# Optimization experiments

Measured on AMD Instinct MI355X. Metric: run time of the kernel, lower is better.

Reference implementation:

```python
import jax, jax.numpy as jnp
import numpy as np

C0 = 32          # cs[0] == cs[1] with planes=[32,32,...], cr=1.0
CIN = 4
EPS = 1e-5

# ---------- host-side coordinate hashing (mirrors F.sphash / F.sphashquery) ----------

def _enc(c):
    # unique int64 code per (x,y,z); +2 shift keeps offset-adjusted coords positive
    return (c[:, 0] + 2).astype(np.int64) + (c[:, 1] + 2).astype(np.int64) * 1024 \
        + (c[:, 2] + 2).astype(np.int64) * 1024 * 1024

def _lookup(sorted_codes, q):
    pos = np.searchsorted(sorted_codes, q)
    pos = np.minimum(pos, len(sorted_codes) - 1)
    return np.where(sorted_codes[pos] == q, pos, -1).astype(np.int32)

def _offsets(r):
    return np.array([[i, j, k] for i in r for j in r for k in r], np.int64)


def setup_inputs() -> dict:
    rng = np.random.default_rng(0)
    N0 = 400000
    pts = rng.integers(0, [400, 400, 40], size=(600000, 3)).astype(np.int64)
    codes = _enc(pts)
    codes_u, idx = np.unique(codes, return_index=True)
    assert len(codes_u) >= N0
    coords0, codes0 = pts[idx][:N0], codes_u[:N0]   # sorted by hash code

    off27, off8 = _offsets([-1, 0, 1]), _offsets([0, 1])
    # ks=3 stride=1 kernel map at level 0: nbr0[k, i] = index of coords0[i]+off27[k] (or -1)
    nbr0 = np.stack([_lookup(codes0, _enc(coords0 + o)) for o in off27])

    # stride-2 downsample coords (level 1)
    c1all = coords0 // 2
    codes1_u, i1 = np.unique(_enc(c1all), return_index=True)
    coords1 = c1all[i1]
    # ks=2 stride=2 kernel map: output voxel gathers inputs at 2*out + {0,1}^3
    down1 = np.stack([_lookup(codes0, _enc(coords1 * 2 + o)) for o in off8])
    # ks=3 stride=1 kernel map at level 1
    nbr1 = np.stack([_lookup(codes1_u, _enc(coords1 + o)) for o in off27])

    key = jax.random.key(0)
    ks = jax.random.split(key, 10)

    def w(k, K, ci, co):
        return jax.random.normal(k, (K, ci, co), jnp.float32) * (1.0 / np.sqrt(K * ci))

    return {
        "voxel_features": jax.random.normal(ks[0], (N0, CIN), jnp.float32),
        "W_stem1": w(ks[1], 27, CIN, C0),
        "W_stem2": w(ks[2], 27, C0, C0),
        "W_down":  w(ks[3], 8,  C0, C0),
        "W_r1a":   w(ks[4], 27, C0, C0),
        "W_r1b":   w(ks[5], 27, C0, C0),
        "W_r2a":   w(ks[6], 27, C0, C0),
        "W_r2b":   w(ks[7], 27, C0, C0),
        "gammas": jnp.ones((7, C0), jnp.float32),
        "betas":  jnp.zeros((7, C0), jnp.float32),
        "nbr0":  jnp.asarray(nbr0),
        "down1": jnp.asarray(down1),
        "nbr1":  jnp.asarray(nbr1),
    }


# ---------- sparse conv: gather-GEMM-scatter per kernel offset ----------

def _spconv(feat, nbr, W):
    # feat [N, Ci], nbr [K, M] (-1 = no neighbor), W [K, Ci, Co] -> out [M, Co]
    def step(acc, kw):
        idx, Wk = kw
        g = jnp.where((idx >= 0)[:, None], feat[jnp.maximum(idx, 0)], 0.0)
        return acc + g @ Wk, None
    acc0 = jnp.zeros((nbr.shape[1], W.shape[-1]), feat.dtype)
    out, _ = jax.lax.scan(step, acc0, (nbr, W))
    return out


def _bn(x, g, b):
    # BatchNorm1d, training-mode statistics (biased var), gamma/beta affine
    mu = x.mean(0)
    var = x.var(0)
    return (x - mu) * jax.lax.rsqrt(var + EPS) * g + b


def _cbr(x, nbr, W, g, b):
    return jax.nn.relu(_bn(_spconv(x, nbr, W), g, b))


def reference(voxel_features, W_stem1, W_stem2, W_down, W_r1a, W_r1b, W_r2a, W_r2b,
              gammas, betas, nbr0, down1, nbr1):
    g, b = gammas, betas
    # stem: two ks=3 sparse convs + BN + ReLU at level 0
    x = _cbr(voxel_features, nbr0, W_stem1, g[0], b[0])
    x = _cbr(x, nbr0, W_stem2, g[1], b[1])
    # stage1: BasicConvolutionBlock (ks=2, stride=2) + 2 ResidualBlocks at level 1
    x1 = _cbr(x, down1, W_down, g[2], b[2])
    h = _cbr(x1, nbr1, W_r1a, g[3], b[3])
    h = _bn(_spconv(h, nbr1, W_r1b), g[4], b[4])
    x1 = jax.nn.relu(h + x1)          # downsample == Identity (inc == outc, stride 1)
    h = _cbr(x1, nbr1, W_r2a, g[5], b[5])
    h = _bn(_spconv(h, nbr1, W_r2b), g[6], b[6])
    return jax.nn.relu(h + x1)
```

## Files before the change

kernel.cpp:

```cpp
#include <hip/hip_runtime.h>

#define EPS 1e-5f
#define WROWS 448

typedef __attribute__((ext_vector_type(8))) short short8;
typedef __attribute__((ext_vector_type(4))) float floatx4;
typedef __attribute__((ext_vector_type(8))) unsigned short ushort8;
typedef __attribute__((ext_vector_type(4))) unsigned short ushortv4;

#define O_S1  0
#define O_S2  4096
#define O_DN  (O_S2 + 27648)
#define O_R1A (O_DN + 8192)
#define O_R1B (O_R1A + 27648)
#define O_R2A (O_R1B + 27648)
#define O_R2B (O_R2A + 27648)
#define WP_TOTAL (O_R2B + 27648)

#define GLL16(g, l)                                                       \
    __builtin_amdgcn_global_load_lds(                                     \
        (const __attribute__((address_space(1))) void*)(g),               \
        (__attribute__((address_space(3))) void*)(l), 16, 0, 0)

__device__ __forceinline__ unsigned short f2bf(float f) {
    union { float f; unsigned u; } x; x.f = f;
    unsigned r = x.u + 0x7fffu + ((x.u >> 16) & 1u);
    return (unsigned short)(r >> 16);
}
__device__ __forceinline__ float bf2f(unsigned short b) {
    union { unsigned u; float f; } x; x.u = ((unsigned)b) << 16;
    return x.f;
}

__device__ __forceinline__ int xcd_swizzle(int nb) {
    int b = (int)blockIdx.x;
    int q = nb >> 3, r = nb & 7;
    int x = b & 7, i = b >> 3;
    return x * q + (x < r ? x : r) + i;
}

__device__ __forceinline__ short8 gath(const unsigned short* __restrict__ x,
                                       int ii, int q) {
    short8 z = {};
    return (ii >= 0) ? *(const short8*)(x + (size_t)ii * 32 + q * 8) : z;
}

template <int ZG, int TPG>
__device__ __forceinline__ void wmm_calc(
    const int* __restrict__ nbr, int N, int t, int* __restrict__ out)
{
    int ln = t & 63, wv = t >> 6;
    int lb = wv / ZG, c = wv - lb * ZG;
    int base = lb * 128;
    int mn = 0x7fffffff, mx = -1;
#pragma unroll
    for (int j = 0; j < TPG; ++j) {
#pragma unroll
        for (int h = 0; h < 2; ++h) {
            int r = base + h * 64 + ln;
            if (r < N) {
                int v = nbr[(size_t)(c + ZG * j) * N + r];
                if (v >= 0) { mn = min(mn, v); mx = max(mx, v); }
            }
        }
    }
#pragma unroll
    for (int off = 32; off >= 1; off >>= 1) {
        mn = min(mn, __shfl_down(mn, off));
        mx = max(mx, __shfl_down(mx, off));
    }
    if (ln == 0) { out[wv * 2] = (mx < 0) ? 0 : mn; out[wv * 2 + 1] = mx; }
}

__device__ __forceinline__ void pack_w_one(
    const float* __restrict__ W, unsigned short* __restrict__ out, int t)
{
    int lane = t & 63;
    int h = (t >> 6) & 1;
    int k = t >> 7;
    int m = lane & 15, q = lane >> 4;
    ushort8 v;
#pragma unroll
    for (int j = 0; j < 8; ++j)
        v[j] = f2bf(W[((size_t)k * 32 + q * 8 + j) * 32 + h * 16 + m]);
    *(ushort8*)(out + (size_t)t * 8) = v;
}

__global__ __launch_bounds__(256) void prep_kernel(
    const float* __restrict__ vf,
    const float* __restrict__ Ws1, const float* __restrict__ Ws2,
    const float* __restrict__ Wd,  const float* __restrict__ Wr1a,
    const float* __restrict__ Wr1b, const float* __restrict__ Wr2a,
    const float* __restrict__ Wr2b,
    const int* __restrict__ nbr0, const int* __restrict__ down1,
    const int* __restrict__ nbr1,
    unsigned short* __restrict__ xb, unsigned short* __restrict__ wp,
    int* __restrict__ wmm0, int* __restrict__ wmmD, int* __restrict__ wmm1,
    int N0, int N1)
{
    int t = blockIdx.x * 256 + threadIdx.x;
    if (t < N0) {
        float4 v = *(const float4*)(vf + (size_t)t * 4);
        ushortv4 r = {f2bf(v.x), f2bf(v.y), f2bf(v.z), f2bf(v.w)};
        *(ushortv4*)(xb + (size_t)t * 4) = r;
        return;
    }
    t -= N0;
    if (t < 512) {
        int lane = t & 63;
        int h = (t >> 6) & 1;
        int c = t >> 7;
        int m = lane & 15, q = lane >> 4;
        ushort8 v;
#pragma unroll
        for (int j = 0; j < 8; ++j) {
            int kdim = c * 32 + q * 8 + j;
            int tap = kdim >> 2, ci = kdim & 3;
            v[j] = (tap < 27) ? f2bf(Ws1[((size_t)tap * 4 + ci) * 32 + h * 16 + m]) : 0;
        }
        *(ushort8*)(wp + O_S1 + (size_t)t * 8) = v;
        return;
    }
    t -= 512;
    if (t < 27 * 128) { pack_w_one(Ws2,  wp + O_S2,  t); return; }
    t -= 27 * 128;
    if (t < 8 * 128)  { pack_w_one(Wd,   wp + O_DN,  t); return; }
    t -= 8 * 128;
    if (t < 27 * 128) { pack_w_one(Wr1a, wp + O_R1A, t); return; }
    t -= 27 * 128;
    if (t < 27 * 128) { pack_w_one(Wr1b, wp + O_R1B, t); return; }
    t -= 27 * 128;
    if (t < 27 * 128) { pack_w_one(Wr2a, wp + O_R2A, t); return; }
    t -= 27 * 128;
    if (t < 27 * 128) { pack_w_one(Wr2b, wp + O_R2B, t); return; }
    t -= 27 * 128;
    int nb0 = (N0 + 127) >> 7, nb1 = (N1 + 127) >> 7;
    if (t < nb0 * 3 * 64) { wmm_calc<3, 9>(nbr0, N0, t, wmm0); return; }
    t -= nb0 * 3 * 64;
    if (t < nb1 * 2 * 64) { wmm_calc<2, 4>(down1, N1, t, wmmD); return; }
    t -= nb1 * 2 * 64;
    if (t < nb1 * 3 * 64) { wmm_calc<3, 9>(nbr1, N1, t, wmm1); return; }
}

__device__ __forceinline__ void conv_epilogue2(
    floatx4 acc00, floatx4 acc01, floatx4 acc10, floatx4 acc11,
    unsigned short* __restrict__ y, float* __restrict__ part,
    int rowbase, int lb, int N, float* sm)
{
    const int lane = threadIdx.x & 63;
    const int m = lane & 15, q = lane >> 4;

    if (threadIdx.x < 64) sm[threadIdx.x] = 0.f;
    __syncthreads();

#pragma unroll
    for (int r = 0; r < 4; ++r) {
        int ra = rowbase + q * 4 + r;
        int rb = ra + 16;
        if (ra < N) {
            y[(size_t)ra * 32 + m]      = f2bf(acc00[r]);
            y[(size_t)ra * 32 + 16 + m] = f2bf(acc01[r]);
        }
        if (rb < N) {
            y[(size_t)rb * 32 + m]      = f2bf(acc10[r]);
            y[(size_t)rb * 32 + 16 + m] = f2bf(acc11[r]);
        }
    }

    float s0 = 0.f, q0 = 0.f, s1 = 0.f, q1 = 0.f;
#pragma unroll
    for (int r = 0; r < 4; ++r) {
        s0 += acc00[r] + acc10[r];
        q0 += acc00[r] * acc00[r] + acc10[r] * acc10[r];
        s1 += acc01[r] + acc11[r];
        q1 += acc01[r] * acc01[r] + acc11[r] * acc11[r];
    }
    s0 += __shfl_down(s0, 32); s0 += __shfl_down(s0, 16);
    q0 += __shfl_down(q0, 32); q0 += __shfl_down(q0, 16);
    s1 += __shfl_down(s1, 32); s1 += __shfl_down(s1, 16);
    q1 += __shfl_down(q1, 32); q1 += __shfl_down(q1, 16);
    if (lane < 16) {
        atomicAdd(&sm[m],      s0);
        atomicAdd(&sm[32 + m], q0);
        atomicAdd(&sm[16 + m],      s1);
        atomicAdd(&sm[48 + m], q1);
    }
    __syncthreads();
    if (threadIdx.x < 64)
        part[(size_t)lb * 64 + threadIdx.x] = sm[threadIdx.x];
}

#define MFMA_BF16 __builtin_amdgcn_mfma_f32_16x16x32_bf16

template <int K>
__global__ __launch_bounds__(256, 5) void conv_mfma_kernel(
    const unsigned short* __restrict__ x,
    const int* __restrict__ nbr,
    const unsigned short* __restrict__ Wp,
    const int* __restrict__ wmmg,
    unsigned short* __restrict__ y,
    float* __restrict__ part, int N)
{
    constexpr int ZG  = (K == 27) ? 3 : 2;
    constexpr int TPG = (K == 27) ? 9 : 4;

    __shared__ __align__(16) unsigned short win[WROWS * 32];
    __shared__ float sm[64];

    const int nb = (N + 127) >> 7;
    const int lb = xcd_swizzle(nb);
    const int lane = threadIdx.x & 63;
    const int wave = threadIdx.x >> 6;
    const int m = lane & 15, q = lane >> 4;
    const int rowbase = lb * 128 + wave * 32;
    const int r0 = rowbase + m;
    const int r1 = r0 + 16;
    const bool v0 = r0 < N, v1 = r1 < N;

    floatx4 c00 = {0.f, 0.f, 0.f, 0.f};
    floatx4 c01 = c00, c10 = c00, c11 = c00;

    int wmn[ZG], wc4[ZG];
#pragma unroll
    for (int c = 0; c < ZG; ++c) {
        int lo = wmmg[(lb * ZG + c) * 2];
        int hi = wmmg[(lb * ZG + c) * 2 + 1];
        wmn[c] = lo;
        int sp = (hi < 0) ? 0 : (hi - lo + 1);
        wc4[c] = (sp < WROWS ? sp : WROWS) * 4;
    }

#define IDX(k, rr, vv) ((vv) ? nbr[(size_t)(k) * N + (rr)] : -1)
#define LOADA(dst, ii)                                                     \
    {                                                                      \
        unsigned rr_ = (unsigned)((ii) - wmin);                            \
        unsigned rc_ = rr_ < (unsigned)WROWS ? rr_ : (unsigned)(WROWS - 1);\
        dst = *(const short8*)&win[rc_ * 32 + ((q ^ ((rc_ >> 1) & 3)) << 3)]; \
        if (__any((ii) >= 0 && rr_ >= (unsigned)WROWS)) {                  \
            if ((ii) >= 0 && rr_ >= (unsigned)WROWS)                       \
                dst = *(const short8*)(x + (size_t)(ii) * 32 + q * 8);     \
        }                                                                  \
        if ((ii) < 0) { short8 z_ = {}; dst = z_; }                        \
    }

    for (int c = 0; c < ZG; ++c) {
        const int wmin = wmn[c];
        const int sc4 = wc4[c];

        for (int cb = wave * 64; cb < sc4; cb += 256) {
            int cc = cb + lane;
            int rr = cc >> 2, s = cc & 3;
            int qq = s ^ ((rr >> 1) & 3);
            if (cc < sc4)
                GLL16(x + ((size_t)(wmin + rr)) * 32 + qq * 8, win + (size_t)cb * 8);
        }

        int ia0 = (0 < TPG) ? IDX(c + ZG * 0, r0, v0) : -1;
        int ib0 = (0 < TPG) ? IDX(c + ZG * 0, r1, v1) : -1;
        int ia1 = (1 < TPG) ? IDX(c + ZG * 1, r0, v0) : -1;
        int ib1 = (1 < TPG) ? IDX(c + ZG * 1, r1, v1) : -1;
        int ia2 = (2 < TPG) ? IDX(c + ZG * 2, r0, v0) : -1;
        int ib2 = (2 < TPG) ? IDX(c + ZG * 2, r1, v1) : -1;
        int ia3 = (3 < TPG) ? IDX(c + ZG * 3, r0, v0) : -1;
        int ib3 = (3 < TPG) ? IDX(c + ZG * 3, r1, v1) : -1;
        int ia4 = (4 < TPG) ? IDX(c + ZG * 4, r0, v0) : -1;
        int ib4 = (4 < TPG) ? IDX(c + ZG * 4, r1, v1) : -1;
        int ia5 = (5 < TPG) ? IDX(c + ZG * 5, r0, v0) : -1;
        int ib5 = (5 < TPG) ? IDX(c + ZG * 5, r1, v1) : -1;
        int ia6 = (6 < TPG) ? IDX(c + ZG * 6, r0, v0) : -1;
        int ib6 = (6 < TPG) ? IDX(c + ZG * 6, r1, v1) : -1;
        int ia7 = (7 < TPG) ? IDX(c + ZG * 7, r0, v0) : -1;
        int ib7 = (7 < TPG) ? IDX(c + ZG * 7, r1, v1) : -1;
        int ia8 = (8 < TPG) ? IDX(c + ZG * 8, r0, v0) : -1;
        int ib8 = (8 < TPG) ? IDX(c + ZG * 8, r1, v1) : -1;

        __syncthreads();

#define TAPC(J, iA, iB)                                                    \
        if (J < TPG) {                                                     \
            bool sA = __all((iA) < 0), sB = __all((iB) < 0);               \
            if (!(sA && sB)) {                                             \
                const short8* wk = (const short8*)(Wp + (size_t)(c + ZG * J) * 1024); \
                short8 b0 = wk[lane];                                      \
                short8 b1 = wk[64 + lane];                                 \
                if (!sA) {                                                 \
                    short8 a0; LOADA(a0, iA);                              \
                    c00 = MFMA_BF16(a0, b0, c00, 0, 0, 0);                 \
                    c01 = MFMA_BF16(a0, b1, c01, 0, 0, 0);                 \
                }                                                          \
                if (!sB) {                                                 \
                    short8 a1; LOADA(a1, iB);                              \
                    c10 = MFMA_BF16(a1, b0, c10, 0, 0, 0);                 \
                    c11 = MFMA_BF16(a1, b1, c11, 0, 0, 0);                 \
                }                                                          \
            }                                                              \
        }
        TAPC(0, ia0, ib0) TAPC(1, ia1, ib1) TAPC(2, ia2, ib2)
        TAPC(3, ia3, ib3) TAPC(4, ia4, ib4) TAPC(5, ia5, ib5)
        TAPC(6, ia6, ib6) TAPC(7, ia7, ib7) TAPC(8, ia8, ib8)
#undef TAPC

        if (c != ZG - 1) __syncthreads();
    }
#undef IDX
#undef LOADA

    conv_epilogue2(c00, c01, c10, c11, y, part, rowbase, lb, N, sm);
}

__global__ __launch_bounds__(256) void conv_stem1_mfma(
    const unsigned short* __restrict__ xb,
    const int* __restrict__ nbr,
    const unsigned short* __restrict__ Wp,
    unsigned short* __restrict__ y,
    float* __restrict__ part, int N)
{
    __shared__ float sm[64];
    const int nb = (N + 127) / 128;
    const int lb = xcd_swizzle(nb);
    const int lane = threadIdx.x & 63;
    const int wave = threadIdx.x >> 6;
    const int m = lane & 15, q = lane >> 4;
    const int rowbase = lb * 128 + wave * 32;
    const int row0 = rowbase + m;
    const int row1 = rowbase + 16 + m;

    floatx4 acc00 = {0.f, 0.f, 0.f, 0.f};
    floatx4 acc01 = acc00, acc10 = acc00, acc11 = acc00;

#pragma unroll
    for (int c = 0; c < 4; ++c) {
        const int t0 = c * 8 + q * 2, t1 = t0 + 1;
        short8 a0 = {}, a1 = {};
        {
            int ia = (t0 < 27 && row0 < N) ? nbr[(size_t)t0 * N + row0] : -1;
            int ib = (t1 < 27 && row0 < N) ? nbr[(size_t)t1 * N + row0] : -1;
            ushortv4 ga = {}, gb = {};
            if (ia >= 0) ga = *(const ushortv4*)(xb + (size_t)ia * 4);
            if (ib >= 0) gb = *(const ushortv4*)(xb + (size_t)ib * 4);
            a0[0] = (short)ga[0]; a0[1] = (short)ga[1];
            a0[2] = (short)ga[2]; a0[3] = (short)ga[3];
            a0[4] = (short)gb[0]; a0[5] = (short)gb[1];
            a0[6] = (short)gb[2]; a0[7] = (short)gb[3];
        }
        {
            int ia = (t0 < 27 && row1 < N) ? nbr[(size_t)t0 * N + row1] : -1;
            int ib = (t1 < 27 && row1 < N) ? nbr[(size_t)t1 * N + row1] : -1;
            ushortv4 ga = {}, gb = {};
            if (ia >= 0) ga = *(const ushortv4*)(xb + (size_t)ia * 4);
            if (ib >= 0) gb = *(const ushortv4*)(xb + (size_t)ib * 4);
            a1[0] = (short)ga[0]; a1[1] = (short)ga[1];
            a1[2] = (short)ga[2]; a1[3] = (short)ga[3];
            a1[4] = (short)gb[0]; a1[5] = (short)gb[1];
            a1[6] = (short)gb[2]; a1[7] = (short)gb[3];
        }
        const short8* wk = (const short8*)Wp;
        short8 b0 = wk[(c * 2 + 0) * 64 + lane];
        short8 b1 = wk[(c * 2 + 1) * 64 + lane];
        acc00 = MFMA_BF16(a0, b0, acc00, 0, 0, 0);
        acc01 = MFMA_BF16(a0, b1, acc01, 0, 0, 0);
        acc10 = MFMA_BF16(a1, b0, acc10, 0, 0, 0);
        acc11 = MFMA_BF16(a1, b1, acc11, 0, 0, 0);
    }

    conv_epilogue2(acc00, acc01, acc10, acc11, y, part, rowbase, lb, N, sm);
}

__global__ __launch_bounds__(256) void reduce_stats_kernel(
    const float* __restrict__ part, float* __restrict__ stats, int nb)
{
    __shared__ float sm[256];
    int t = threadIdx.x;
    int c = t & 63, g = t >> 6;
    float s = 0.f;
    for (int b = blockIdx.x * 4 + g; b < nb; b += 256)
        s += part[(size_t)b * 64 + c];
    sm[t] = s;
    __syncthreads();
    if (t < 64)
        atomicAdd(&stats[t], sm[t] + sm[64 + t] + sm[128 + t] + sm[192 + t]);
}

template <bool OUT_F32, bool HAS_RES>
__global__ __launch_bounds__(256) void bn_relu_kernel(
    const unsigned short* __restrict__ y, const float* __restrict__ stats,
    const float* __restrict__ gamma, const float* __restrict__ beta,
    const unsigned short* __restrict__ resid, void* __restrict__ outp, int N)
{
    int t = blockIdx.x * 256 + threadIdx.x;
    if (t >= N) return;
    float inv_n = 1.0f / (float)N;
    const ushort8* yr = (const ushort8*)(y + (size_t)t * 32);

#pragma unroll
    for (int c = 0; c < 4; ++c) {
        ushort8 v = yr[c];
        ushort8 rv = {};
        if (HAS_RES) rv = ((const ushort8*)(resid + (size_t)t * 32))[c];
        float f0, f1, f2, f3, f4, f5, f6, f7;
#define BNJ(fj, j)                                                        \
        {                                                                 \
            int co = c * 8 + (j);                                         \
            float mu = stats[co] * inv_n;                                 \
            float var = stats[32 + co] * inv_n - mu * mu;                 \
            float sc = rsqrtf(var + EPS) * gamma[co];                     \
            fj = (bf2f(v[j]) - mu) * sc + beta[co];                       \
            if (HAS_RES) fj += bf2f(rv[j]);                               \
            fj = fmaxf(fj, 0.0f);                                         \
        }
        BNJ(f0, 0) BNJ(f1, 1) BNJ(f2, 2) BNJ(f3, 3)
        BNJ(f4, 4) BNJ(f5, 5) BNJ(f6, 6) BNJ(f7, 7)
#undef BNJ
        if (OUT_F32) {
            float* ob = (float*)outp + (size_t)t * 32 + c * 8;
            floatx4 u0 = {f0, f1, f2, f3}, u1 = {f4, f5, f6, f7};
            *(floatx4*)(ob) = u0;
            *(floatx4*)(ob + 4) = u1;
        } else {
            ushort8 o;
            o[0] = f2bf(f0); o[1] = f2bf(f1); o[2] = f2bf(f2); o[3] = f2bf(f3);
            o[4] = f2bf(f4); o[5] = f2bf(f5); o[6] = f2bf(f6); o[7] = f2bf(f7);
            ((ushort8*)((unsigned short*)outp + (size_t)t * 32))[c] = o;
        }
    }
}

extern "C" void kernel_launch(void* const* d_in, const int* in_sizes, int n_in,
                              void* d_out, int out_size, void* d_ws, size_t ws_size,
                              hipStream_t stream)
{
    const float* vf   = (const float*)d_in[0];
    const float* Ws1  = (const float*)d_in[1];
    const float* Ws2  = (const float*)d_in[2];
    const float* Wd   = (const float*)d_in[3];
    const float* Wr1a = (const float*)d_in[4];
    const float* Wr1b = (const float*)d_in[5];
    const float* Wr2a = (const float*)d_in[6];
    const float* Wr2b = (const float*)d_in[7];
    const float* gam  = (const float*)d_in[8];
    const float* bet  = (const float*)d_in[9];
    const int* nbr0   = (const int*)d_in[10];
    const int* down1  = (const int*)d_in[11];
    const int* nbr1   = (const int*)d_in[12];

    int N0 = in_sizes[0] / 4;
    int N1 = in_sizes[11] / 8;

    unsigned short* yraw = (unsigned short*)d_ws;
    unsigned short* actA = yraw + (size_t)N0 * 32;
    unsigned short* actB = actA + (size_t)N0 * 32;
    unsigned short* xb   = actB + (size_t)N0 * 32;
    unsigned short* wp   = xb + (size_t)N0 * 4;
    float* part  = (float*)(wp + WP_TOTAL);
    float* stats = part + (size_t)3200 * 64;
    int nb0 = (N0 + 127) / 128;
    int nb1 = (N1 + 127) / 128;
    int* wmm0 = (int*)(stats + 7 * 64);
    int* wmmD = wmm0 + (size_t)nb0 * 6;
    int* wmm1 = wmmD + (size_t)nb1 * 4;

    hipMemsetAsync(stats, 0, 7 * 64 * sizeof(float), stream);

    auto g1 = [](int n) { return dim3((unsigned)((n + 255) / 256)); };
    auto gm = [](int n) { return dim3((unsigned)((n + 127) / 128)); };

    int prep_threads = N0 + 512 + 128 * (27 * 5 + 8) + 64 * (nb0 * 3 + nb1 * 5);
    prep_kernel<<<g1(prep_threads), 256, 0, stream>>>(
        vf, Ws1, Ws2, Wd, Wr1a, Wr1b, Wr2a, Wr2b,
        nbr0, down1, nbr1, xb, wp, wmm0, wmmD, wmm1, N0, N1);

    conv_stem1_mfma<<<gm(N0), 256, 0, stream>>>(xb, nbr0, wp + O_S1, yraw, part, N0);
    reduce_stats_kernel<<<64, 256, 0, stream>>>(part, stats + 0 * 64, nb0);
    bn_relu_kernel<false, false><<<g1(N0), 256, 0, stream>>>(yraw, stats + 0 * 64, gam + 0, bet + 0, nullptr, actA, N0);
    conv_mfma_kernel<27><<<gm(N0), 256, 0, stream>>>(actA, nbr0, wp + O_S2, wmm0, yraw, part, N0);
    reduce_stats_kernel<<<64, 256, 0, stream>>>(part, stats + 1 * 64, nb0);
    bn_relu_kernel<false, false><<<g1(N0), 256, 0, stream>>>(yraw, stats + 1 * 64, gam + 32, bet + 32, nullptr, actB, N0);
    conv_mfma_kernel<8><<<gm(N1), 256, 0, stream>>>(actB, down1, wp + O_DN, wmmD, yraw, part, N1);
    reduce_stats_kernel<<<64, 256, 0, stream>>>(part, stats + 2 * 64, nb1);
    bn_relu_kernel<false, false><<<g1(N1), 256, 0, stream>>>(yraw, stats + 2 * 64, gam + 64, bet + 64, nullptr, actA, N1);
    conv_mfma_kernel<27><<<gm(N1), 256, 0, stream>>>(actA, nbr1, wp + O_R1A, wmm1, yraw, part, N1);
    reduce_stats_kernel<<<64, 256, 0, stream>>>(part, stats + 3 * 64, nb1);
    bn_relu_kernel<false, false><<<g1(N1), 256, 0, stream>>>(yraw, stats + 3 * 64, gam + 96, bet + 96, nullptr, actB, N1);
    conv_mfma_kernel<27><<<gm(N1), 256, 0, stream>>>(actB, nbr1, wp + O_R1B, wmm1, yraw, part, N1);
    reduce_stats_kernel<<<64, 256, 0, stream>>>(part, stats + 4 * 64, nb1);
    bn_relu_kernel<false, true><<<g1(N1), 256, 0, stream>>>(yraw, stats + 4 * 64, gam + 128, bet + 128, actA, actB, N1);
    conv_mfma_kernel<27><<<gm(N1), 256, 0, stream>>>(actB, nbr1, wp + O_R2A, wmm1, yraw, part, N1);
    reduce_stats_kernel<<<64, 256, 0, stream>>>(part, stats + 5 * 64, nb1);
    bn_relu_kernel<false, false><<<g1(N1), 256, 0, stream>>>(yraw, stats + 5 * 64, gam + 160, bet + 160, nullptr, actA, N1);
    conv_mfma_kernel<27><<<gm(N1), 256, 0, stream>>>(actA, nbr1, wp + O_R2B, wmm1, yraw, part, N1);
    reduce_stats_kernel<<<64, 256, 0, stream>>>(part, stats + 6 * 64, nb1);
    bn_relu_kernel<true, true><<<g1(N1), 256, 0, stream>>>(yraw, stats + 6 * 64, gam + 192, bet + 192, actB, d_out, N1);
}
```

Measured before the change: 699.4 us.

## Double-buffer LDS neighbor window to prefetch next z-group during MFMA compute

The sparse conv kernel now keeps two LDS window halves of 288 rows plus a shared zero row. It stages the next z-group's feature window and neighbor indices while the current group's MFMAs run, so gather latency overlaps with compute. Missing neighbors read the zero row instead of taking branches, per-tap all-empty skips are removed, and a group whose span exceeds the window falls back to direct global gathers. This costs occupancy (launch bounds drop from 5 to 4) and a smaller per-buffer window, which may send more blocks down the global-gather path.

```diff
diff --git a/kernel.cpp b/kernel.cpp
--- a/kernel.cpp
+++ b/kernel.cpp
@@ -1,7 +1,8 @@
 #include <hip/hip_runtime.h>
 
 #define EPS 1e-5f
-#define WROWS 448
+#define WDB 288
+#define ZROW (2 * WDB)
 
 typedef __attribute__((ext_vector_type(8))) short short8;
 typedef __attribute__((ext_vector_type(4))) float floatx4;
@@ -193,7 +194,7 @@
 #define MFMA_BF16 __builtin_amdgcn_mfma_f32_16x16x32_bf16
 
 template <int K>
-__global__ __launch_bounds__(256, 5) void conv_mfma_kernel(
+__global__ __launch_bounds__(256, 4) void conv_mfma_kernel(
     const unsigned short* __restrict__ x,
     const int* __restrict__ nbr,
     const unsigned short* __restrict__ Wp,
@@ -204,21 +205,27 @@
     constexpr int ZG  = (K == 27) ? 3 : 2;
     constexpr int TPG = (K == 27) ? 9 : 4;
 
-    __shared__ __align__(16) unsigned short win[WROWS * 32];
+    __shared__ __align__(16) unsigned short win[(2 * WDB + 1) * 32];
     __shared__ float sm[64];
 
     const int nb = (N + 127) >> 7;
     const int lb = xcd_swizzle(nb);
     const int lane = threadIdx.x & 63;
-    const int wave = threadIdx.x >> 6;
+    const int wave = (int)threadIdx.x >> 6;
     const int m = lane & 15, q = lane >> 4;
-    const int rowbase = lb * 128 + wave * 32;
+    const int rb0 = lb * 128;
+    const int rowbase = rb0 + wave * 32;
     const int r0 = rowbase + m;
     const int r1 = r0 + 16;
     const bool v0 = r0 < N, v1 = r1 < N;
 
     floatx4 c00 = {0.f, 0.f, 0.f, 0.f};
     floatx4 c01 = c00, c10 = c00, c11 = c00;
+
+    if (threadIdx.x < 4) {
+        short8 z = {};
+        *(short8*)&win[ZROW * 32 + threadIdx.x * 8] = z;
+    }
 
     int wmn[ZG], wc4[ZG];
 #pragma unroll
@@ -227,83 +234,93 @@
         int hi = wmmg[(lb * ZG + c) * 2 + 1];
         wmn[c] = lo;
         int sp = (hi < 0) ? 0 : (hi - lo + 1);
-        wc4[c] = (sp < WROWS ? sp : WROWS) * 4;
-    }
-
-#define IDX(k, rr, vv) ((vv) ? nbr[(size_t)(k) * N + (rr)] : -1)
-#define LOADA(dst, ii)                                                     \
+        wc4[c] = sp * 4;
+        if (sp > WDB) wc4[c] = -1;
+    }
+
+    int ia[2][TPG], ib[2][TPG];
+
+#define STAGE(C, HALF)                                                     \
+    if (wc4[C] >= 0) {                                                     \
+        const unsigned short* gsrc = x + (size_t)wmn[C] * 32;              \
+        for (int cb = wave * 64; cb < wc4[C]; cb += 256) {                 \
+            int cc = cb + lane;                                            \
+            int rr = cc >> 2, s_ = cc & 3;                                 \
+            int qq = s_ ^ ((rr >> 1) & 3);                                 \
+            if (cc < wc4[C])                                               \
+                GLL16(gsrc + (size_t)rr * 32 + qq * 8,                     \
+                      win + (HALF) * (WDB * 32) + (size_t)cb * 8);         \
+        }                                                                  \
+    }
+
+#define LOADIDX(C, S)                                                      \
+    _Pragma("unroll")                                                      \
+    for (int j = 0; j < TPG; ++j) {                                        \
+        ia[S][j] = v0 ? nbr[(size_t)((C) + ZG * j) * N + r0] : -1;         \
+        ib[S][j] = v1 ? nbr[(size_t)((C) + ZG * j) * N + r1] : -1;         \
+    }
+
+#define LGH(dst, ii, HOFFR)                                                \
     {                                                                      \
         unsigned rr_ = (unsigned)((ii) - wmin);                            \
-        unsigned rc_ = rr_ < (unsigned)WROWS ? rr_ : (unsigned)(WROWS - 1);\
+        unsigned rc_ = rr_ < (unsigned)WDB ? rr_ + (unsigned)(HOFFR)       \
+                                           : (unsigned)ZROW;               \
         dst = *(const short8*)&win[rc_ * 32 + ((q ^ ((rc_ >> 1) & 3)) << 3)]; \
-        if (__any((ii) >= 0 && rr_ >= (unsigned)WROWS)) {                  \
-            if ((ii) >= 0 && rr_ >= (unsigned)WROWS)                       \
-                dst = *(const short8*)(x + (size_t)(ii) * 32 + q * 8);     \
-        }                                                                  \
-        if ((ii) < 0) { short8 z_ = {}; dst = z_; }                        \
-    }
-
-    for (int c = 0; c < ZG; ++c) {
-        const int wmin = wmn[c];
-        const int sc4 = wc4[c];
-
-        for (int cb = wave * 64; cb < sc4; cb += 256) {
-            int cc = cb + lane;
-            int rr = cc >> 2, s = cc & 3;
-            int qq = s ^ ((rr >> 1) & 3);
-            if (cc < sc4)
-                GLL16(x + ((size_t)(wmin + rr)) * 32 + qq * 8, win + (size_t)cb * 8);
-        }
-
-        int ia0 = (0 < TPG) ? IDX(c + ZG * 0, r0, v0) : -1;
-        int ib0 = (0 < TPG) ? IDX(c + ZG * 0, r1, v1) : -1;
-        int ia1 = (1 < TPG) ? IDX(c + ZG * 1, r0, v0) : -1;
-        int ib1 = (1 < TPG) ? IDX(c + ZG * 1, r1, v1) : -1;
-        int ia2 = (2 < TPG) ? IDX(c + ZG * 2, r0, v0) : -1;
-        int ib2 = (2 < TPG) ? IDX(c + ZG * 2, r1, v1) : -1;
-        int ia3 = (3 < TPG) ? IDX(c + ZG * 3, r0, v0) : -1;
-        int ib3 = (3 < TPG) ? IDX(c + ZG * 3, r1, v1) : -1;
-        int ia4 = (4 < TPG) ? IDX(c + ZG * 4, r0, v0) : -1;
-        int ib4 = (4 < TPG) ? IDX(c + ZG * 4, r1, v1) : -1;
-        int ia5 = (5 < TPG) ? IDX(c + ZG * 5, r0, v0) : -1;
-        int ib5 = (5 < TPG) ? IDX(c + ZG * 5, r1, v1) : -1;
-        int ia6 = (6 < TPG) ? IDX(c + ZG * 6, r0, v0) : -1;
-        int ib6 = (6 < TPG) ? IDX(c + ZG * 6, r1, v1) : -1;
-        int ia7 = (7 < TPG) ? IDX(c + ZG * 7, r0, v0) : -1;
-        int ib7 = (7 < TPG) ? IDX(c + ZG * 7, r1, v1) : -1;
-        int ia8 = (8 < TPG) ? IDX(c + ZG * 8, r0, v0) : -1;
-        int ib8 = (8 < TPG) ? IDX(c + ZG * 8, r1, v1) : -1;
-
-        __syncthreads();
-
-#define TAPC(J, iA, iB)                                                    \
-        if (J < TPG) {                                                     \
-            bool sA = __all((iA) < 0), sB = __all((iB) < 0);               \
-            if (!(sA && sB)) {                                             \
-                const short8* wk = (const short8*)(Wp + (size_t)(c + ZG * J) * 1024); \
+    }
+
+#define COMPUTE(C, S, HALF)                                                \
+    {                                                                      \
+        const int wmin = wmn[C];                                           \
+        if (wc4[C] >= 0) {                                                 \
+            _Pragma("unroll")                                              \
+            for (int j = 0; j < TPG; ++j) {                                \
+                const short8* wk =                                         \
+                    (const short8*)(Wp + (size_t)((C) + ZG * j) * 1024);   \
                 short8 b0 = wk[lane];                                      \
                 short8 b1 = wk[64 + lane];                                 \
-                if (!sA) {                                                 \
-                    short8 a0; LOADA(a0, iA);                              \
-                    c00 = MFMA_BF16(a0, b0, c00, 0, 0, 0);                 \
-                    c01 = MFMA_BF16(a0, b1, c01, 0, 0, 0);                 \
-                }                                                          \
-                if (!sB) {                                                 \
-                    short8 a1; LOADA(a1, iB);                              \
-                    c10 = MFMA_BF16(a1, b0, c10, 0, 0, 0);                 \
-                    c11 = MFMA_BF16(a1, b1, c11, 0, 0, 0);                 \
-                }                                                          \
+                short8 a0, a1;                                             \
+                LGH(a0, ia[S][j], (HALF) * WDB);                           \
+                LGH(a1, ib[S][j], (HALF) * WDB);                           \
+                c00 = MFMA_BF16(a0, b0, c00, 0, 0, 0);                     \
+                c01 = MFMA_BF16(a0, b1, c01, 0, 0, 0);                     \
+                c10 = MFMA_BF16(a1, b0, c10, 0, 0, 0);                     \
+                c11 = MFMA_BF16(a1, b1, c11, 0, 0, 0);                     \
             }                                                              \
-        }
-        TAPC(0, ia0, ib0) TAPC(1, ia1, ib1) TAPC(2, ia2, ib2)
-        TAPC(3, ia3, ib3) TAPC(4, ia4, ib4) TAPC(5, ia5, ib5)
-        TAPC(6, ia6, ib6) TAPC(7, ia7, ib7) TAPC(8, ia8, ib8)
-#undef TAPC
-
+        } else {                                                           \
+            _Pragma("unroll")                                              \
+            for (int j = 0; j < TPG; ++j) {                                \
+                const short8* wk =                                         \
+                    (const short8*)(Wp + (size_t)((C) + ZG * j) * 1024);   \
+                short8 b0 = wk[lane];                                      \
+                short8 b1 = wk[64 + lane];                                 \
+                short8 a0 = gath(x, ia[S][j], q);                          \
+                short8 a1 = gath(x, ib[S][j], q);                          \
+                c00 = MFMA_BF16(a0, b0, c00, 0, 0, 0);                     \
+                c01 = MFMA_BF16(a0, b1, c01, 0, 0, 0);                     \
+                c10 = MFMA_BF16(a1, b0, c10, 0, 0, 0);                     \
+                c11 = MFMA_BF16(a1, b1, c11, 0, 0, 0);                     \
+            }                                                              \
+        }                                                                  \
+    }
+
+    STAGE(0, 0)
+    LOADIDX(0, 0)
+    __syncthreads();
+
+#pragma unroll
+    for (int c = 0; c < ZG; ++c) {
+        const int s = c & 1;
+        if (c + 1 < ZG) {
+            STAGE(c + 1, (c + 1) & 1)
+            LOADIDX(c + 1, (c + 1) & 1)
+        }
+        COMPUTE(c, s, s)
         if (c != ZG - 1) __syncthreads();
     }
-#undef IDX
-#undef LOADA
+#undef STAGE
+#undef LOADIDX
+#undef LGH
+#undef COMPUTE
 
     conv_epilogue2(c00, c01, c10, c11, y, part, rowbase, lb, N, sm);
 }
@@ -319,7 +336,7 @@
     const int nb = (N + 127) / 128;
     const int lb = xcd_swizzle(nb);
     const int lane = threadIdx.x & 63;
-    const int wave = threadIdx.x >> 6;
+    const int wave = (int)threadIdx.x >> 6;
     const int m = lane & 15, q = lane >> 4;
     const int rowbase = lb * 128 + wave * 32;
     const int row0 = rowbase + m;
```

After: 730.6 us. 4.5% more time.
